# Kernel optimization log

Measured on AMD Instinct MI355X. Metric: run time of the kernel, lower is better.

The kernel has to match this reference:

```python
import jax, jax.numpy as jnp
import numpy as np

TAU = 2.0
BN_EPS = 1e-5
SG_ALPHA = 4.0  # spikingjelly default sigmoid surrogate alpha

@jax.custom_vjp
def heaviside(x):
    return (x >= 0).astype(x.dtype)

def _h_fwd(x):
    return heaviside(x), x

def _h_bwd(x, g):
    sg = jax.nn.sigmoid(SG_ALPHA * x)
    return (SG_ALPHA * sg * (1.0 - sg) * g,)

heaviside.defvjp(_h_fwd, _h_bwd)

def lif(x, v_th):
    # x: (T, ...). LIFNode defaults: tau=2, decay_input=True, v_reset=0 (hard reset).
    def step(v, xt):
        v = v + (xt - v) / TAU
        s = heaviside(v - v_th)
        return v * (1.0 - s), s
    _, spikes = jax.lax.scan(step, jnp.zeros_like(x[0]), x)
    return spikes

def bn(x, gamma, beta, mean, var):
    # x: (T,B,D,V), channel axis = 2; inference-mode BatchNorm1d
    inv = gamma * jax.lax.rsqrt(var + BN_EPS)
    return x * inv[None, None, :, None] + (beta - mean * inv)[None, None, :, None]

def conv1x1(W, x):
    # W: (out,in), x: (T,B,D,V)
    return jnp.einsum('od,tbdv->tbov', W, x)

def setup_inputs() -> dict:
    key = jax.random.key(0)
    T, B, D, V = 4, 64, 512, 256
    ks = jax.random.split(key, 4)
    s = 1.0 / np.sqrt(D)
    return {
        'x': jax.random.normal(ks[0], (T, B, D, V), jnp.float32),
        'Wq': jax.random.normal(ks[1], (D, D), jnp.float32) * s,
        'q_gamma': jnp.ones((D,), jnp.float32), 'q_beta': jnp.zeros((D,), jnp.float32),
        'q_mean': jnp.zeros((D,), jnp.float32), 'q_var': jnp.ones((D,), jnp.float32),
        'Wk': jax.random.normal(ks[2], (D, D), jnp.float32) * s,
        'k_gamma': jnp.ones((D,), jnp.float32), 'k_beta': jnp.zeros((D,), jnp.float32),
        'k_mean': jnp.zeros((D,), jnp.float32), 'k_var': jnp.ones((D,), jnp.float32),
        'Wp': jax.random.normal(ks[3], (D, D), jnp.float32) * s,
        'p_gamma': jnp.ones((D,), jnp.float32), 'p_beta': jnp.zeros((D,), jnp.float32),
        'p_mean': jnp.zeros((D,), jnp.float32), 'p_var': jnp.ones((D,), jnp.float32),
    }

def reference(x, Wq, q_gamma, q_beta, q_mean, q_var,
              Wk, k_gamma, k_beta, k_mean, k_var,
              Wp, p_gamma, p_beta, p_mean, p_var):
    T, B, D, V = x.shape
    H = 4
    hd = D // H
    q = lif(bn(conv1x1(Wq, x), q_gamma, q_beta, q_mean, q_var), 1.0)
    k = lif(bn(conv1x1(Wk, x), k_gamma, k_beta, k_mean, k_var), 1.0)
    qh = q.reshape(T, B, H, hd, V)
    kh = k.reshape(T, B, H, hd, V)
    q_sum = qh.sum(axis=3, keepdims=True)        # (T,B,H,1,V)
    gate = lif(q_sum, 0.5)                        # attn_lif, threshold 0.5
    out = (gate * kh).reshape(T, B, D, V)
    out2 = lif(bn(conv1x1(Wp, out), p_gamma, p_beta, p_mean, p_var), 1.0)
    return out2
```

## Files before the change

kernel.cpp:

```cpp
#include <hip/hip_runtime.h>

#define T_ 4
#define B_ 64
#define D_ 512
#define V_ 256

#define XSH   0ull
#define XSM   67108864ull
#define XSL   134217728ull
#define OUTBT 201326592ull
#define WT    268435456ull
#define BNOF  273154048ull

typedef unsigned short u16;
typedef __attribute__((ext_vector_type(8))) __bf16 bf16x8;
typedef __attribute__((ext_vector_type(4))) float f32x4;
typedef __attribute__((ext_vector_type(8))) unsigned short u16x8;
typedef __attribute__((ext_vector_type(4))) unsigned short u16x4;

__device__ __forceinline__ u16 f2bf(float f) {
    unsigned u = __float_as_uint(f);
    return (u16)((u + 0x7FFFu + ((u >> 16) & 1u)) >> 16);
}
__device__ __forceinline__ float bf2f(u16 h) {
    return __uint_as_float(((unsigned)h) << 16);
}

__global__ __launch_bounds__(256) void k_prep2(
    const float* __restrict__ Wq, const float* __restrict__ Wk, const float* __restrict__ Wp,
    const float* __restrict__ qg, const float* __restrict__ qb,
    const float* __restrict__ qm, const float* __restrict__ qv,
    const float* __restrict__ kg, const float* __restrict__ kb,
    const float* __restrict__ km, const float* __restrict__ kv,
    const float* __restrict__ pg, const float* __restrict__ pb,
    const float* __restrict__ pm, const float* __restrict__ pv,
    char* __restrict__ ws)
{
    const int g = blockIdx.x * 256 + threadIdx.x;
    const int mat = g >> 15;
    const int r = g & 32767;
    const int lane = r & 63;
    const int q = r >> 6;
    const int ip = q & 7;
    const int q2 = q >> 3;
    const int it = q2 & 15;
    const int head = q2 >> 4;
    const int row = head * 128 + ip * 16 + (lane & 15);
    const int kcol = it * 32 + (lane >> 4) * 8;
    const float* W = (mat == 0) ? Wq : (mat == 1 ? Wk : Wp);

    u16x8 h8, m8, l8;
#pragma unroll
    for (int e = 0; e < 8; ++e) {
        const float f = W[row * 512 + kcol + e];
        const u16 h = f2bf(f);          const float fh = bf2f(h);
        const u16 m = f2bf(f - fh);     const float fm = bf2f(m);
        const u16 l = f2bf(f - fh - fm);
        h8[e] = h; m8[e] = m; l8[e] = l;
    }
    u16* wt = (u16*)(ws + WT);
    const size_t o = (size_t)r * 8;
    *(u16x8*)(wt + (size_t)(mat * 3 + 0) * 262144 + o) = h8;
    *(u16x8*)(wt + (size_t)(mat * 3 + 1) * 262144 + o) = m8;
    *(u16x8*)(wt + (size_t)(mat * 3 + 2) * 262144 + o) = l8;

    if (g < 512) {
        float* bn = (float*)(ws + BNOF);
        float iv;
        iv = qg[g] * (1.0f / sqrtf(qv[g] + 1e-5f)); bn[g]        = iv; bn[512  + g] = qb[g] - qm[g] * iv;
        iv = kg[g] * (1.0f / sqrtf(kv[g] + 1e-5f)); bn[1024 + g] = iv; bn[1536 + g] = kb[g] - km[g] * iv;
        iv = pg[g] * (1.0f / sqrtf(pv[g] + 1e-5f)); bn[2048 + g] = iv; bn[2560 + g] = pb[g] - pm[g] * iv;
    }
}

__global__ __launch_bounds__(256) void k_split_x2(
    const float* __restrict__ x, char* __restrict__ ws)
{
    const int bt = blockIdx.x >> 4;
    const int it = blockIdx.x & 15;
    const int tid = threadIdx.x;
#pragma unroll
    for (int r2 = 0; r2 < 4; ++r2) {
        const int slot = r2 * 256 + tid;
        const int vg = slot >> 6;
        const int ll = slot & 63;
        const int v  = vg * 16 + (ll & 15);
        const int d0 = it * 32 + (ll >> 4) * 8;
        u16x8 h8, m8, l8;
#pragma unroll
        for (int e = 0; e < 8; ++e) {
            const float f = x[(size_t)bt * 131072 + (size_t)(d0 + e) * 256 + v];
            const u16 h = f2bf(f);          const float fh = bf2f(h);
            const u16 m = f2bf(f - fh);     const float fm = bf2f(m);
            const u16 lo = f2bf(f - fh - fm);
            h8[e] = h; m8[e] = m; l8[e] = lo;
        }
        const size_t o = (size_t)bt * 262144ull + (size_t)it * 16384ull
                       + (size_t)vg * 1024ull + (size_t)ll * 16ull;
        *(u16x8*)(ws + XSH + o) = h8;
        *(u16x8*)(ws + XSM + o) = m8;
        *(u16x8*)(ws + XSL + o) = l8;
    }
}

__global__ __launch_bounds__(512, 2) void k_qk2(char* __restrict__ ws)
{
    __shared__ u16 tile[32768];
    __shared__ float qs[2][256];
    __shared__ float gatef[4][256];

    const int tid  = threadIdx.x;
    const int lane = tid & 63;
    const int wave = tid >> 6;
    const int wr = wave >> 2;
    const int wc = wave & 3;
    const int quad = lane >> 4;
    const int l15  = lane & 15;

    const int xcd  = blockIdx.x & 7;
    const int slot = blockIdx.x >> 3;
    const int b    = xcd * 8 + (slot >> 2);
    const int head = slot & 3;

    constexpr int PA[6] = {0, 0, 1, 1, 0, 2};
    constexpr int PB[6] = {0, 1, 0, 1, 2, 0};

    float gstate = 0.f;

    for (int ph = 0; ph < 2; ++ph) {
        const size_t abase = WT + (size_t)ph * 3ull * 524288ull
                           + (size_t)head * 131072ull
                           + (size_t)wr * 4096ull + (size_t)lane * 16ull;
        const float* bn = (const float*)(ws + BNOF + (size_t)ph * 4096);

        f32x4 st[4][4];
#pragma unroll
        for (int i = 0; i < 4; ++i)
#pragma unroll
            for (int j = 0; j < 4; ++j) st[i][j] = (f32x4){0.f, 0.f, 0.f, 0.f};

        for (int t = 0; t < 4; ++t) {
            const int bt = t * 64 + b;
            const size_t bbase = (size_t)bt * 262144ull
                               + (size_t)(wc * 4) * 1024ull + (size_t)lane * 16ull;
            f32x4 acc[4][4];
#pragma unroll
            for (int i = 0; i < 4; ++i)
#pragma unroll
                for (int j = 0; j < 4; ++j) acc[i][j] = (f32x4){0.f, 0.f, 0.f, 0.f};

#pragma unroll 4
            for (int it = 0; it < 16; ++it) {
                bf16x8 afr[3][4];
#pragma unroll
                for (int s = 0; s < 3; ++s)
#pragma unroll
                    for (int i = 0; i < 4; ++i)
                        afr[s][i] = *(const bf16x8*)(ws + abase + (size_t)s * 524288ull
                                      + (size_t)it * 8192ull + (size_t)i * 1024ull);
#pragma unroll
                for (int j = 0; j < 4; ++j) {
                    bf16x8 bfr[3];
#pragma unroll
                    for (int s = 0; s < 3; ++s)
                        bfr[s] = *(const bf16x8*)(ws + (size_t)s * 67108864ull + bbase
                                   + (size_t)it * 16384ull + (size_t)j * 1024ull);
#pragma unroll
                    for (int i = 0; i < 4; ++i)
#pragma unroll
                        for (int p = 0; p < 6; ++p)
                            acc[i][j] = __builtin_amdgcn_mfma_f32_16x16x32_bf16(
                                afr[PA[p]][i], bfr[PB[p]], acc[i][j], 0, 0, 0);
                }
            }

            if (ph == 0) {
                float qp[4] = {0.f, 0.f, 0.f, 0.f};
#pragma unroll
                for (int i = 0; i < 4; ++i) {
                    const int ob = head * 128 + wr * 64 + i * 16 + quad * 4;
                    const f32x4 inv = *(const f32x4*)(bn + ob);
                    const f32x4 add = *(const f32x4*)(bn + 512 + ob);
#pragma unroll
                    for (int j = 0; j < 4; ++j)
#pragma unroll
                        for (int r = 0; r < 4; ++r) {
                            const float y = acc[i][j][r] * inv[r] + add[r];
                            float v = (st[i][j][r] + y) * 0.5f;
                            const float s = (v >= 1.0f) ? 1.f : 0.f;
                            st[i][j][r] = (v >= 1.0f) ? 0.f : v;
                            qp[j] += s;
                        }
                }
#pragma unroll
                for (int j = 0; j < 4; ++j) {
                    qp[j] += __shfl_xor(qp[j], 16, 64);
                    qp[j] += __shfl_xor(qp[j], 32, 64);
                }
                if (quad == 0) {
#pragma unroll
                    for (int j = 0; j < 4; ++j)
                        qs[wr][wc * 64 + j * 16 + l15] = qp[j];
                }
                __syncthreads();
                if (tid < 256) {
                    const float qsum = qs[0][tid] + qs[1][tid];
                    gstate = (gstate + qsum) * 0.5f;
                    const float gt = (gstate >= 0.5f) ? 1.f : 0.f;
                    gstate = (gstate >= 0.5f) ? 0.f : gstate;
                    gatef[t][tid] = gt;
                }
                __syncthreads();
            } else {
#pragma unroll
                for (int i = 0; i < 4; ++i) {
                    const int ob = head * 128 + wr * 64 + i * 16 + quad * 4;
                    const f32x4 inv = *(const f32x4*)(bn + ob);
                    const f32x4 add = *(const f32x4*)(bn + 512 + ob);
                    const int itL = wr * 2 + (i >> 1);
                    const int ls  = ((i & 1) * 2 + (quad >> 1)) * 16 + l15;
                    const int e0  = (quad & 1) * 4;
#pragma unroll
                    for (int j = 0; j < 4; ++j) {
                        const int col = wc * 64 + j * 16 + l15;
                        const float gt = gatef[t][col];
                        u16x4 w;
#pragma unroll
                        for (int r = 0; r < 4; ++r) {
                            const float y = acc[i][j][r] * inv[r] + add[r];
                            float v = (st[i][j][r] + y) * 0.5f;
                            const float s = (v >= 1.0f) ? 1.f : 0.f;
                            st[i][j][r] = (v >= 1.0f) ? 0.f : v;
                            w[r] = (s * gt != 0.f) ? (u16)0x3F80 : (u16)0;
                        }
                        *(u16x4*)&tile[(size_t)((itL * 16 + wc * 4 + j) * 64 + ls) * 8 + e0] = w;
                    }
                }
                __syncthreads();
                const size_t dst = OUTBT + ((size_t)bt * 16ull + (size_t)head * 4ull) * 16384ull;
#pragma unroll
                for (int c = 0; c < 8; ++c) {
                    const int idx = c * 512 + tid;
                    *(float4*)(ws + dst + (size_t)idx * 16) = *(const float4*)&tile[(size_t)idx * 8];
                }
                __syncthreads();
            }
        }
    }
}

__global__ __launch_bounds__(512, 2) void k_p2(char* __restrict__ ws,
                                               float* __restrict__ out2)
{
    const int tid  = threadIdx.x;
    const int lane = tid & 63;
    const int wave = tid >> 6;
    const int wr = wave >> 2;
    const int wc = wave & 3;
    const int quad = lane >> 4;
    const int l15  = lane & 15;

    const int xcd  = blockIdx.x & 7;
    const int slot = blockIdx.x >> 3;
    const int b  = xcd * 8 + (slot >> 2);
    const int ot = slot & 3;

    const size_t abase = WT + 6ull * 524288ull + (size_t)ot * 131072ull
                       + (size_t)wr * 4096ull + (size_t)lane * 16ull;
    const float* bn = (const float*)(ws + BNOF + 8192);

    f32x4 st[4][4];
#pragma unroll
    for (int i = 0; i < 4; ++i)
#pragma unroll
        for (int j = 0; j < 4; ++j) st[i][j] = (f32x4){0.f, 0.f, 0.f, 0.f};

    for (int t = 0; t < 4; ++t) {
        const int bt = t * 64 + b;
        const size_t bbase = OUTBT + (size_t)bt * 262144ull
                           + (size_t)(wc * 4) * 1024ull + (size_t)lane * 16ull;
        f32x4 acc[4][4];
#pragma unroll
        for (int i = 0; i < 4; ++i)
#pragma unroll
            for (int j = 0; j < 4; ++j) acc[i][j] = (f32x4){0.f, 0.f, 0.f, 0.f};

#pragma unroll 4
        for (int it = 0; it < 16; ++it) {
            bf16x8 afr[3][4];
#pragma unroll
            for (int s = 0; s < 3; ++s)
#pragma unroll
                for (int i = 0; i < 4; ++i)
                    afr[s][i] = *(const bf16x8*)(ws + abase + (size_t)s * 524288ull
                                  + (size_t)it * 8192ull + (size_t)i * 1024ull);
#pragma unroll
            for (int j = 0; j < 4; ++j) {
                const bf16x8 bfr = *(const bf16x8*)(ws + bbase
                                     + (size_t)it * 16384ull + (size_t)j * 1024ull);
#pragma unroll
                for (int i = 0; i < 4; ++i)
#pragma unroll
                    for (int p = 0; p < 3; ++p)
                        acc[i][j] = __builtin_amdgcn_mfma_f32_16x16x32_bf16(
                            afr[p][i], bfr, acc[i][j], 0, 0, 0);
            }
        }

#pragma unroll
        for (int i = 0; i < 4; ++i) {
            const int ob = ot * 128 + wr * 64 + i * 16 + quad * 4;
            const f32x4 inv = *(const f32x4*)(bn + ob);
            const f32x4 add = *(const f32x4*)(bn + 512 + ob);
#pragma unroll
            for (int j = 0; j < 4; ++j) {
                const int col = wc * 64 + j * 16 + l15;
#pragma unroll
                for (int r = 0; r < 4; ++r) {
                    const float y = acc[i][j][r] * inv[r] + add[r];
                    float v = (st[i][j][r] + y) * 0.5f;
                    const float s = (v >= 1.0f) ? 1.f : 0.f;
                    st[i][j][r] = (v >= 1.0f) ? 0.f : v;
                    out2[((size_t)(t * 64 + b) * 512 + ob + r) * 256 + col] = s;
                }
            }
        }
    }
}

extern "C" void kernel_launch(void* const* d_in, const int* in_sizes, int n_in,
                              void* d_out, int out_size, void* d_ws, size_t ws_size,
                              hipStream_t stream)
{
    const float* x  = (const float*)d_in[0];
    const float* Wq = (const float*)d_in[1];
    const float* qg = (const float*)d_in[2];
    const float* qb = (const float*)d_in[3];
    const float* qm = (const float*)d_in[4];
    const float* qv = (const float*)d_in[5];
    const float* Wk = (const float*)d_in[6];
    const float* kg = (const float*)d_in[7];
    const float* kb = (const float*)d_in[8];
    const float* km = (const float*)d_in[9];
    const float* kv = (const float*)d_in[10];
    const float* Wp = (const float*)d_in[11];
    const float* pg = (const float*)d_in[12];
    const float* pb = (const float*)d_in[13];
    const float* pm = (const float*)d_in[14];
    const float* pv = (const float*)d_in[15];

    char* ws = (char*)d_ws;

    k_prep2<<<384, 256, 0, stream>>>(Wq, Wk, Wp, qg, qb, qm, qv,
                                     kg, kb, km, kv, pg, pb, pm, pv, ws);

    k_split_x2<<<4096, 256, 0, stream>>>(x, ws);

    k_qk2<<<256, 512, 0, stream>>>(ws);

    k_p2<<<256, 512, 0, stream>>>(ws, (float*)d_out);
}
```

Before: 711.4 us.

## Process two timesteps per pass to reuse weight fragments across GEMMs

Both fused GEMM kernels now handle timesteps in pairs. Each weight (A) fragment loaded from global memory feeds MFMAs for two timesteps' activations, which halves weight reloads and gives more independent MFMA chains. The cost is a second 4x4 accumulator set, roughly doubling accumulator registers, which could cause spills or lower occupancy under launch_bounds(512,2). The unroll factor drops from 4 to 2 to compensate, and the LIF epilogues still run sequentially per timestep.

```diff
diff --git a/kernel.cpp b/kernel.cpp
--- a/kernel.cpp
+++ b/kernel.cpp
@@ -139,17 +139,98 @@
 #pragma unroll
             for (int j = 0; j < 4; ++j) st[i][j] = (f32x4){0.f, 0.f, 0.f, 0.f};
 
-        for (int t = 0; t < 4; ++t) {
-            const int bt = t * 64 + b;
-            const size_t bbase = (size_t)bt * 262144ull
-                               + (size_t)(wc * 4) * 1024ull + (size_t)lane * 16ull;
-            f32x4 acc[4][4];
+        auto epi_q = [&](int t, f32x4 (&acc)[4][4]) {
+            float qp[4] = {0.f, 0.f, 0.f, 0.f};
+#pragma unroll
+            for (int i = 0; i < 4; ++i) {
+                const int ob = head * 128 + wr * 64 + i * 16 + quad * 4;
+                const f32x4 inv = *(const f32x4*)(bn + ob);
+                const f32x4 add = *(const f32x4*)(bn + 512 + ob);
+#pragma unroll
+                for (int j = 0; j < 4; ++j)
+#pragma unroll
+                    for (int r = 0; r < 4; ++r) {
+                        const float y = acc[i][j][r] * inv[r] + add[r];
+                        float v = (st[i][j][r] + y) * 0.5f;
+                        const float s = (v >= 1.0f) ? 1.f : 0.f;
+                        st[i][j][r] = (v >= 1.0f) ? 0.f : v;
+                        qp[j] += s;
+                    }
+            }
+#pragma unroll
+            for (int j = 0; j < 4; ++j) {
+                qp[j] += __shfl_xor(qp[j], 16, 64);
+                qp[j] += __shfl_xor(qp[j], 32, 64);
+            }
+            if (quad == 0) {
+#pragma unroll
+                for (int j = 0; j < 4; ++j)
+                    qs[wr][wc * 64 + j * 16 + l15] = qp[j];
+            }
+            __syncthreads();
+            if (tid < 256) {
+                const float qsum = qs[0][tid] + qs[1][tid];
+                gstate = (gstate + qsum) * 0.5f;
+                const float gt = (gstate >= 0.5f) ? 1.f : 0.f;
+                gstate = (gstate >= 0.5f) ? 0.f : gstate;
+                gatef[t][tid] = gt;
+            }
+            __syncthreads();
+        };
+
+        auto epi_k = [&](int t, int bt, f32x4 (&acc)[4][4]) {
+#pragma unroll
+            for (int i = 0; i < 4; ++i) {
+                const int ob = head * 128 + wr * 64 + i * 16 + quad * 4;
+                const f32x4 inv = *(const f32x4*)(bn + ob);
+                const f32x4 add = *(const f32x4*)(bn + 512 + ob);
+                const int itL = wr * 2 + (i >> 1);
+                const int ls  = ((i & 1) * 2 + (quad >> 1)) * 16 + l15;
+                const int e0  = (quad & 1) * 4;
+#pragma unroll
+                for (int j = 0; j < 4; ++j) {
+                    const int col = wc * 64 + j * 16 + l15;
+                    const float gt = gatef[t][col];
+                    u16x4 w;
+#pragma unroll
+                    for (int r = 0; r < 4; ++r) {
+                        const float y = acc[i][j][r] * inv[r] + add[r];
+                        float v = (st[i][j][r] + y) * 0.5f;
+                        const float s = (v >= 1.0f) ? 1.f : 0.f;
+                        st[i][j][r] = (v >= 1.0f) ? 0.f : v;
+                        w[r] = (s * gt != 0.f) ? (u16)0x3F80 : (u16)0;
+                    }
+                    *(u16x4*)&tile[(size_t)((itL * 16 + wc * 4 + j) * 64 + ls) * 8 + e0] = w;
+                }
+            }
+            __syncthreads();
+            const size_t dst = OUTBT + ((size_t)bt * 16ull + (size_t)head * 4ull) * 16384ull;
+#pragma unroll
+            for (int c = 0; c < 8; ++c) {
+                const int idx = c * 512 + tid;
+                *(float4*)(ws + dst + (size_t)idx * 16) = *(const float4*)&tile[(size_t)idx * 8];
+            }
+            __syncthreads();
+        };
+
+        for (int tp = 0; tp < 2; ++tp) {
+            const int ta = tp * 2, tb = tp * 2 + 1;
+            const int bta = ta * 64 + b, btb = tb * 64 + b;
+            const size_t bbaseA = (size_t)bta * 262144ull
+                                + (size_t)(wc * 4) * 1024ull + (size_t)lane * 16ull;
+            const size_t bbaseB = (size_t)btb * 262144ull
+                                + (size_t)(wc * 4) * 1024ull + (size_t)lane * 16ull;
+
+            f32x4 acc0[4][4], acc1[4][4];
 #pragma unroll
             for (int i = 0; i < 4; ++i)
 #pragma unroll
-                for (int j = 0; j < 4; ++j) acc[i][j] = (f32x4){0.f, 0.f, 0.f, 0.f};
-
-#pragma unroll 4
+                for (int j = 0; j < 4; ++j) {
+                    acc0[i][j] = (f32x4){0.f, 0.f, 0.f, 0.f};
+                    acc1[i][j] = (f32x4){0.f, 0.f, 0.f, 0.f};
+                }
+
+#pragma unroll 2
             for (int it = 0; it < 16; ++it) {
                 bf16x8 afr[3][4];
 #pragma unroll
@@ -160,90 +241,32 @@
                                       + (size_t)it * 8192ull + (size_t)i * 1024ull);
 #pragma unroll
                 for (int j = 0; j < 4; ++j) {
-                    bf16x8 bfr[3];
-#pragma unroll
-                    for (int s = 0; s < 3; ++s)
-                        bfr[s] = *(const bf16x8*)(ws + (size_t)s * 67108864ull + bbase
+                    bf16x8 b0[3], b1[3];
+#pragma unroll
+                    for (int s = 0; s < 3; ++s) {
+                        b0[s] = *(const bf16x8*)(ws + (size_t)s * 67108864ull + bbaseA
                                    + (size_t)it * 16384ull + (size_t)j * 1024ull);
+                        b1[s] = *(const bf16x8*)(ws + (size_t)s * 67108864ull + bbaseB
+                                   + (size_t)it * 16384ull + (size_t)j * 1024ull);
+                    }
 #pragma unroll
                     for (int i = 0; i < 4; ++i)
 #pragma unroll
-                        for (int p = 0; p < 6; ++p)
-                            acc[i][j] = __builtin_amdgcn_mfma_f32_16x16x32_bf16(
-                                afr[PA[p]][i], bfr[PB[p]], acc[i][j], 0, 0, 0);
-                }
-            }
-
-            if (ph == 0) {
-                float qp[4] = {0.f, 0.f, 0.f, 0.f};
-#pragma unroll
-                for (int i = 0; i < 4; ++i) {
-                    const int ob = head * 128 + wr * 64 + i * 16 + quad * 4;
-                    const f32x4 inv = *(const f32x4*)(bn + ob);
-                    const f32x4 add = *(const f32x4*)(bn + 512 + ob);
-#pragma unroll
-                    for (int j = 0; j < 4; ++j)
-#pragma unroll
-                        for (int r = 0; r < 4; ++r) {
-                            const float y = acc[i][j][r] * inv[r] + add[r];
-                            float v = (st[i][j][r] + y) * 0.5f;
-                            const float s = (v >= 1.0f) ? 1.f : 0.f;
-                            st[i][j][r] = (v >= 1.0f) ? 0.f : v;
-                            qp[j] += s;
+                        for (int p = 0; p < 6; ++p) {
+                            acc0[i][j] = __builtin_amdgcn_mfma_f32_16x16x32_bf16(
+                                afr[PA[p]][i], b0[PB[p]], acc0[i][j], 0, 0, 0);
+                            acc1[i][j] = __builtin_amdgcn_mfma_f32_16x16x32_bf16(
+                                afr[PA[p]][i], b1[PB[p]], acc1[i][j], 0, 0, 0);
                         }
                 }
-#pragma unroll
-                for (int j = 0; j < 4; ++j) {
-                    qp[j] += __shfl_xor(qp[j], 16, 64);
-                    qp[j] += __shfl_xor(qp[j], 32, 64);
-                }
-                if (quad == 0) {
-#pragma unroll
-                    for (int j = 0; j < 4; ++j)
-                        qs[wr][wc * 64 + j * 16 + l15] = qp[j];
-                }
-                __syncthreads();
-                if (tid < 256) {
-                    const float qsum = qs[0][tid] + qs[1][tid];
-                    gstate = (gstate + qsum) * 0.5f;
-                    const float gt = (gstate >= 0.5f) ? 1.f : 0.f;
-                    gstate = (gstate >= 0.5f) ? 0.f : gstate;
-                    gatef[t][tid] = gt;
-                }
-                __syncthreads();
+            }
+
+            if (ph == 0) {
+                epi_q(ta, acc0);
+                epi_q(tb, acc1);
             } else {
-#pragma unroll
-                for (int i = 0; i < 4; ++i) {
-                    const int ob = head * 128 + wr * 64 + i * 16 + quad * 4;
-                    const f32x4 inv = *(const f32x4*)(bn + ob);
-                    const f32x4 add = *(const f32x4*)(bn + 512 + ob);
-                    const int itL = wr * 2 + (i >> 1);
-                    const int ls  = ((i & 1) * 2 + (quad >> 1)) * 16 + l15;
-                    const int e0  = (quad & 1) * 4;
-#pragma unroll
-                    for (int j = 0; j < 4; ++j) {
-                        const int col = wc * 64 + j * 16 + l15;
-                        const float gt = gatef[t][col];
-                        u16x4 w;
-#pragma unroll
-                        for (int r = 0; r < 4; ++r) {
-                            const float y = acc[i][j][r] * inv[r] + add[r];
-                            float v = (st[i][j][r] + y) * 0.5f;
-                            const float s = (v >= 1.0f) ? 1.f : 0.f;
-                            st[i][j][r] = (v >= 1.0f) ? 0.f : v;
-                            w[r] = (s * gt != 0.f) ? (u16)0x3F80 : (u16)0;
-                        }
-                        *(u16x4*)&tile[(size_t)((itL * 16 + wc * 4 + j) * 64 + ls) * 8 + e0] = w;
-                    }
-                }
-                __syncthreads();
-                const size_t dst = OUTBT + ((size_t)bt * 16ull + (size_t)head * 4ull) * 16384ull;
-#pragma unroll
-                for (int c = 0; c < 8; ++c) {
-                    const int idx = c * 512 + tid;
-                    *(float4*)(ws + dst + (size_t)idx * 16) = *(const float4*)&tile[(size_t)idx * 8];
-                }
-                __syncthreads();
+                epi_k(ta, bta, acc0);
+                epi_k(tb, btb, acc1);
             }
         }
     }
@@ -275,38 +298,7 @@
 #pragma unroll
         for (int j = 0; j < 4; ++j) st[i][j] = (f32x4){0.f, 0.f, 0.f, 0.f};
 
-    for (int t = 0; t < 4; ++t) {
-        const int bt = t * 64 + b;
-        const size_t bbase = OUTBT + (size_t)bt * 262144ull
-                           + (size_t)(wc * 4) * 1024ull + (size_t)lane * 16ull;
-        f32x4 acc[4][4];
-#pragma unroll
-        for (int i = 0; i < 4; ++i)
-#pragma unroll
-            for (int j = 0; j < 4; ++j) acc[i][j] = (f32x4){0.f, 0.f, 0.f, 0.f};
-
-#pragma unroll 4
-        for (int it = 0; it < 16; ++it) {
-            bf16x8 afr[3][4];
-#pragma unroll
-            for (int s = 0; s < 3; ++s)
-#pragma unroll
-                for (int i = 0; i < 4; ++i)
-                    afr[s][i] = *(const bf16x8*)(ws + abase + (size_t)s * 524288ull
-                                  + (size_t)it * 8192ull + (size_t)i * 1024ull);
-#pragma unroll
-            for (int j = 0; j < 4; ++j) {
-                const bf16x8 bfr = *(const bf16x8*)(ws + bbase
-                                     + (size_t)it * 16384ull + (size_t)j * 1024ull);
-#pragma unroll
-                for (int i = 0; i < 4; ++i)
-#pragma unroll
-                    for (int p = 0; p < 3; ++p)
-                        acc[i][j] = __builtin_amdgcn_mfma_f32_16x16x32_bf16(
-                            afr[p][i], bfr, acc[i][j], 0, 0, 0);
-            }
-        }
-
+    auto epi = [&](int t, f32x4 (&acc)[4][4]) {
 #pragma unroll
         for (int i = 0; i < 4; ++i) {
             const int ob = ot * 128 + wr * 64 + i * 16 + quad * 4;
@@ -325,6 +317,54 @@
                 }
             }
         }
+    };
+
+    for (int tp = 0; tp < 2; ++tp) {
+        const int ta = tp * 2, tb = tp * 2 + 1;
+        const int bta = ta * 64 + b, btb = tb * 64 + b;
+        const size_t bbaseA = OUTBT + (size_t)bta * 262144ull
+                            + (size_t)(wc * 4) * 1024ull + (size_t)lane * 16ull;
+        const size_t bbaseB = OUTBT + (size_t)btb * 262144ull
+                            + (size_t)(wc * 4) * 1024ull + (size_t)lane * 16ull;
+
+        f32x4 acc0[4][4], acc1[4][4];
+#pragma unroll
+        for (int i = 0; i < 4; ++i)
+#pragma unroll
+            for (int j = 0; j < 4; ++j) {
+                acc0[i][j] = (f32x4){0.f, 0.f, 0.f, 0.f};
+                acc1[i][j] = (f32x4){0.f, 0.f, 0.f, 0.f};
+            }
+
+#pragma unroll 2
+        for (int it = 0; it < 16; ++it) {
+            bf16x8 afr[3][4];
+#pragma unroll
+            for (int s = 0; s < 3; ++s)
+#pragma unroll
+                for (int i = 0; i < 4; ++i)
+                    afr[s][i] = *(const bf16x8*)(ws + abase + (size_t)s * 524288ull
+                                  + (size_t)it * 8192ull + (size_t)i * 1024ull);
+#pragma unroll
+            for (int j = 0; j < 4; ++j) {
+                const bf16x8 b0 = *(const bf16x8*)(ws + bbaseA
+                                     + (size_t)it * 16384ull + (size_t)j * 1024ull);
+                const bf16x8 b1 = *(const bf16x8*)(ws + bbaseB
+                                     + (size_t)it * 16384ull + (size_t)j * 1024ull);
+#pragma unroll
+                for (int i = 0; i < 4; ++i)
+#pragma unroll
+                    for (int p = 0; p < 3; ++p) {
+                        acc0[i][j] = __builtin_amdgcn_mfma_f32_16x16x32_bf16(
+                            afr[p][i], b0, acc0[i][j], 0, 0, 0);
+                        acc1[i][j] = __builtin_amdgcn_mfma_f32_16x16x32_bf16(
+                            afr[p][i], b1, acc1[i][j], 0, 0, 0);
+                    }
+            }
+        }
+
+        epi(ta, acc0);
+        epi(tb, acc1);
     }
 }
 
```

Result: slower. 750.4 us (+5.5%).

## Stage GEMM operands through double-buffered LDS with async global-to-LDS loads

Applied to the files above, without the earlier changes.

Both GEMM kernels now stage weight and activation tiles into shared memory using global_load_lds direct loads, double-buffered so the next k-slice is fetched while the current one feeds MFMA. Previously each wave loaded fragments straight from global memory, so the same data was re-read by several waves with no cross-wave reuse. The large LDS footprint forces occupancy down to one block per CU and adds two barriers per iteration, which could limit latency hiding.

```diff
diff --git a/kernel.cpp b/kernel.cpp
--- a/kernel.cpp
+++ b/kernel.cpp
@@ -25,6 +25,11 @@
 __device__ __forceinline__ float bf2f(u16 h) {
     return __uint_as_float(((unsigned)h) << 16);
 }
+
+#define GLL16(g, l) __builtin_amdgcn_global_load_lds( \
+    (const __attribute__((address_space(1))) void*)(g), \
+    (__attribute__((address_space(3))) void*)(l), 16, 0, 0)
+#define WAITVM(n) asm volatile("s_waitcnt vmcnt(" #n ")" ::: "memory")
 
 __global__ __launch_bounds__(256) void k_prep2(
     const float* __restrict__ Wq, const float* __restrict__ Wk, const float* __restrict__ Wp,
@@ -103,11 +108,12 @@
     }
 }
 
-__global__ __launch_bounds__(512, 2) void k_qk2(char* __restrict__ ws)
+__global__ __launch_bounds__(512, 1) void k_qk2(char* __restrict__ ws)
 {
-    __shared__ u16 tile[32768];
-    __shared__ float qs[2][256];
-    __shared__ float gatef[4][256];
+    __shared__ char lds[153600];
+    u16*   tile  = (u16*)lds;
+    float* qs    = (float*)(lds + 147456);
+    float* gatef = (float*)(lds + 149504);
 
     const int tid  = threadIdx.x;
     const int lane = tid & 63;
@@ -116,6 +122,7 @@
     const int wc = wave & 3;
     const int quad = lane >> 4;
     const int l15  = lane & 15;
+    const int to   = tid * 16;
 
     const int xcd  = blockIdx.x & 7;
     const int slot = blockIdx.x >> 3;
@@ -128,9 +135,7 @@
     float gstate = 0.f;
 
     for (int ph = 0; ph < 2; ++ph) {
-        const size_t abase = WT + (size_t)ph * 3ull * 524288ull
-                           + (size_t)head * 131072ull
-                           + (size_t)wr * 4096ull + (size_t)lane * 16ull;
+        const size_t wbase = WT + (size_t)ph * 3ull * 524288ull + (size_t)head * 131072ull;
         const float* bn = (const float*)(ws + BNOF + (size_t)ph * 4096);
 
         f32x4 st[4][4];
@@ -141,30 +146,61 @@
 
         for (int t = 0; t < 4; ++t) {
             const int bt = t * 64 + b;
-            const size_t bbase = (size_t)bt * 262144ull
-                               + (size_t)(wc * 4) * 1024ull + (size_t)lane * 16ull;
+            const size_t btbase = (size_t)bt * 262144ull;
+
             f32x4 acc[4][4];
 #pragma unroll
             for (int i = 0; i < 4; ++i)
 #pragma unroll
                 for (int j = 0; j < 4; ++j) acc[i][j] = (f32x4){0.f, 0.f, 0.f, 0.f};
 
-#pragma unroll 4
+#pragma unroll
+            for (int s = 0; s < 3; ++s)
+                GLL16(ws + wbase + (size_t)s * 524288ull + to,
+                      lds + s * 8192 + to);
+#pragma unroll
+            for (int s = 0; s < 3; ++s)
+#pragma unroll
+                for (int h = 0; h < 2; ++h)
+                    GLL16(ws + (size_t)s * 67108864ull + btbase + h * 8192 + to,
+                          lds + 24576 + s * 16384 + h * 8192 + to);
+
+#pragma unroll 2
             for (int it = 0; it < 16; ++it) {
+                char* buf = lds + (it & 1) * 73728;
+                if (it < 15) {
+                    char* nbuf = lds + ((it + 1) & 1) * 73728;
+                    const size_t itn = (size_t)(it + 1);
+#pragma unroll
+                    for (int s = 0; s < 3; ++s)
+                        GLL16(ws + wbase + (size_t)s * 524288ull + itn * 8192ull + to,
+                              nbuf + s * 8192 + to);
+#pragma unroll
+                    for (int s = 0; s < 3; ++s)
+#pragma unroll
+                        for (int h = 0; h < 2; ++h)
+                            GLL16(ws + (size_t)s * 67108864ull + btbase + itn * 16384ull + h * 8192 + to,
+                                  nbuf + 24576 + s * 16384 + h * 8192 + to);
+                    WAITVM(9);
+                } else {
+                    WAITVM(0);
+                }
+                __builtin_amdgcn_s_barrier();
+
                 bf16x8 afr[3][4];
 #pragma unroll
                 for (int s = 0; s < 3; ++s)
 #pragma unroll
                     for (int i = 0; i < 4; ++i)
-                        afr[s][i] = *(const bf16x8*)(ws + abase + (size_t)s * 524288ull
-                                      + (size_t)it * 8192ull + (size_t)i * 1024ull);
+                        afr[s][i] = *(const bf16x8*)(buf + s * 8192 + wr * 4096
+                                                     + i * 1024 + lane * 16);
 #pragma unroll
                 for (int j = 0; j < 4; ++j) {
                     bf16x8 bfr[3];
 #pragma unroll
                     for (int s = 0; s < 3; ++s)
-                        bfr[s] = *(const bf16x8*)(ws + (size_t)s * 67108864ull + bbase
-                                   + (size_t)it * 16384ull + (size_t)j * 1024ull);
+                        bfr[s] = *(const bf16x8*)(buf + 24576 + s * 16384
+                                                  + (wc * 4 + j) * 1024 + lane * 16);
 #pragma unroll
                     for (int i = 0; i < 4; ++i)
 #pragma unroll
@@ -172,6 +208,7 @@
                             acc[i][j] = __builtin_amdgcn_mfma_f32_16x16x32_bf16(
                                 afr[PA[p]][i], bfr[PB[p]], acc[i][j], 0, 0, 0);
                 }
+                __builtin_amdgcn_s_barrier();
             }
 
             if (ph == 0) {
@@ -200,15 +237,15 @@
                 if (quad == 0) {
 #pragma unroll
                     for (int j = 0; j < 4; ++j)
-                        qs[wr][wc * 64 + j * 16 + l15] = qp[j];
+                        qs[wr * 256 + wc * 64 + j * 16 + l15] = qp[j];
                 }
                 __syncthreads();
                 if (tid < 256) {
-                    const float qsum = qs[0][tid] + qs[1][tid];
+                    const float qsum = qs[tid] + qs[256 + tid];
                     gstate = (gstate + qsum) * 0.5f;
                     const float gt = (gstate >= 0.5f) ? 1.f : 0.f;
                     gstate = (gstate >= 0.5f) ? 0.f : gstate;
-                    gatef[t][tid] = gt;
+                    gatef[t * 256 + tid] = gt;
                 }
                 __syncthreads();
             } else {
@@ -223,7 +260,7 @@
 #pragma unroll
                     for (int j = 0; j < 4; ++j) {
                         const int col = wc * 64 + j * 16 + l15;
-                        const float gt = gatef[t][col];
+                        const float gt = gatef[t * 256 + col];
                         u16x4 w;
 #pragma unroll
                         for (int r = 0; r < 4; ++r) {
@@ -249,9 +286,11 @@
     }
 }
 
-__global__ __launch_bounds__(512, 2) void k_p2(char* __restrict__ ws,
+__global__ __launch_bounds__(512, 1) void k_p2(char* __restrict__ ws,
                                                float* __restrict__ out2)
 {
+    __shared__ char lds[81920];
+
     const int tid  = threadIdx.x;
     const int lane = tid & 63;
     const int wave = tid >> 6;
@@ -259,14 +298,14 @@
     const int wc = wave & 3;
     const int quad = lane >> 4;
     const int l15  = lane & 15;
+    const int to   = tid * 16;
 
     const int xcd  = blockIdx.x & 7;
     const int slot = blockIdx.x >> 3;
     const int b  = xcd * 8 + (slot >> 2);
     const int ot = slot & 3;
 
-    const size_t abase = WT + 6ull * 524288ull + (size_t)ot * 131072ull
-                       + (size_t)wr * 4096ull + (size_t)lane * 16ull;
+    const size_t wbase = WT + 6ull * 524288ull + (size_t)ot * 131072ull;
     const float* bn = (const float*)(ws + BNOF + 8192);
 
     f32x4 st[4][4];
@@ -277,27 +316,54 @@
 
     for (int t = 0; t < 4; ++t) {
         const int bt = t * 64 + b;
-        const size_t bbase = OUTBT + (size_t)bt * 262144ull
-                           + (size_t)(wc * 4) * 1024ull + (size_t)lane * 16ull;
+        const size_t btbase = OUTBT + (size_t)bt * 262144ull;
+
         f32x4 acc[4][4];
 #pragma unroll
         for (int i = 0; i < 4; ++i)
 #pragma unroll
             for (int j = 0; j < 4; ++j) acc[i][j] = (f32x4){0.f, 0.f, 0.f, 0.f};
 
-#pragma unroll 4
+#pragma unroll
+        for (int s = 0; s < 3; ++s)
+            GLL16(ws + wbase + (size_t)s * 524288ull + to,
+                  lds + s * 8192 + to);
+#pragma unroll
+        for (int h = 0; h < 2; ++h)
+            GLL16(ws + btbase + h * 8192 + to,
+                  lds + 24576 + h * 8192 + to);
+
+#pragma unroll 2
         for (int it = 0; it < 16; ++it) {
+            char* buf = lds + (it & 1) * 40960;
+            if (it < 15) {
+                char* nbuf = lds + ((it + 1) & 1) * 40960;
+                const size_t itn = (size_t)(it + 1);
+#pragma unroll
+                for (int s = 0; s < 3; ++s)
+                    GLL16(ws + wbase + (size_t)s * 524288ull + itn * 8192ull + to,
+                          nbuf + s * 8192 + to);
+#pragma unroll
+                for (int h = 0; h < 2; ++h)
+                    GLL16(ws + btbase + itn * 16384ull + h * 8192 + to,
+                          nbuf + 24576 + h * 8192 + to);
+                WAITVM(5);
+            } else {
+                WAITVM(0);
+            }
+            __builtin_amdgcn_s_barrier();
+
             bf16x8 afr[3][4];
 #pragma unroll
             for (int s = 0; s < 3; ++s)
 #pragma unroll
                 for (int i = 0; i < 4; ++i)
-                    afr[s][i] = *(const bf16x8*)(ws + abase + (size_t)s * 524288ull
-                                  + (size_t)it * 8192ull + (size_t)i * 1024ull);
+                    afr[s][i] = *(const bf16x8*)(buf + s * 8192 + wr * 4096
+                                                 + i * 1024 + lane * 16);
 #pragma unroll
             for (int j = 0; j < 4; ++j) {
-                const bf16x8 bfr = *(const bf16x8*)(ws + bbase
-                                     + (size_t)it * 16384ull + (size_t)j * 1024ull);
+                const bf16x8 bfr = *(const bf16x8*)(buf + 24576
+                                                    + (wc * 4 + j) * 1024 + lane * 16);
 #pragma unroll
                 for (int i = 0; i < 4; ++i)
 #pragma unroll
@@ -305,6 +371,7 @@
                         acc[i][j] = __builtin_amdgcn_mfma_f32_16x16x32_bf16(
                             afr[p][i], bfr, acc[i][j], 0, 0, 0);
             }
+            __builtin_amdgcn_s_barrier();
         }
 
 #pragma unroll
@@ -325,6 +392,7 @@
                 }
             }
         }
+        WAITVM(0);
     }
 }
 
```

After: 656.7 us. -7.7%, faster.

## Stage GEMM operands through double-buffered LDS with async global-to-LDS loads

Applied to the files above, without the earlier changes.

Both GEMM kernels now copy A (weights) and B (activations) tiles into LDS with global_load_lds. The buffers are double-buffered, so the next K-step's loads are issued while the current step's MFMAs run, replacing direct per-wave global loads. Coordination uses vmcnt waits, raw s_barrier and setprio around MFMA blocks. The q/k output tile is written straight to global instead of staged through LDS. The larger LDS footprint drops occupancy to one block per CU, and correctness now depends on hand-tuned waitcnt counts.

```diff
diff --git a/kernel.cpp b/kernel.cpp
--- a/kernel.cpp
+++ b/kernel.cpp
@@ -25,6 +25,12 @@
 __device__ __forceinline__ float bf2f(u16 h) {
     return __uint_as_float(((unsigned)h) << 16);
 }
+
+#define GLL16(g, l) __builtin_amdgcn_global_load_lds( \
+    (const __attribute__((address_space(1))) void*)(g), \
+    (__attribute__((address_space(3))) void*)(l), 16, 0, 0)
+#define WAITVM(n) asm volatile("s_waitcnt vmcnt(" #n ")" ::: "memory")
+#define WAITLGKM() asm volatile("s_waitcnt lgkmcnt(0)" ::: "memory")
 
 __global__ __launch_bounds__(256) void k_prep2(
     const float* __restrict__ Wq, const float* __restrict__ Wk, const float* __restrict__ Wp,
@@ -103,11 +109,11 @@
     }
 }
 
-__global__ __launch_bounds__(512, 2) void k_qk2(char* __restrict__ ws)
+__global__ __launch_bounds__(512, 1) void k_qk2(char* __restrict__ ws)
 {
-    __shared__ u16 tile[32768];
-    __shared__ float qs[2][256];
-    __shared__ float gatef[4][256];
+    __shared__ char lds[150528];
+    float* qs    = (float*)(lds + 147456);
+    float* gatef = (float*)(lds + 149504);
 
     const int tid  = threadIdx.x;
     const int lane = tid & 63;
@@ -116,6 +122,9 @@
     const int wc = wave & 3;
     const int quad = lane >> 4;
     const int l15  = lane & 15;
+    const int to   = tid * 16;
+    const int offB0 = (wc * 4 + 0 + wr) * 1024 + lane * 16;
+    const int offB1 = (wc * 4 + 2 + wr) * 1024 + lane * 16;
 
     const int xcd  = blockIdx.x & 7;
     const int slot = blockIdx.x >> 3;
@@ -125,55 +134,81 @@
     constexpr int PA[6] = {0, 0, 1, 1, 0, 2};
     constexpr int PB[6] = {0, 1, 0, 1, 2, 0};
 
+#define QK_ISSUE_A(gg, nb) { \
+    const size_t wb_ = WT + (size_t)((gg) >> 6) * 1572864ull \
+                     + (size_t)head * 131072ull + (size_t)((gg) & 15) * 8192ull; \
+    _Pragma("unroll") \
+    for (int s_ = 0; s_ < 3; ++s_) \
+        GLL16(ws + wb_ + (size_t)s_ * 524288ull + to, (nb) + s_ * 8192 + to); }
+
+#define QK_ISSUE_B(gg, nb, off) { \
+    const size_t bb_ = (size_t)(((((gg) >> 4) & 3) * 64 + b)) * 262144ull \
+                     + (size_t)((gg) & 15) * 16384ull; \
+    _Pragma("unroll") \
+    for (int s_ = 0; s_ < 3; ++s_) \
+        GLL16(ws + (size_t)s_ * 67108864ull + bb_ + (off), (nb) + 24576 + s_ * 16384 + (off)); }
+
+#define QK_DO_J(jq) { \
+    bf16x8 bfr[3]; \
+    _Pragma("unroll") \
+    for (int s_ = 0; s_ < 3; ++s_) \
+        bfr[s_] = *(const bf16x8*)(buf + 24576 + s_ * 16384 + (wc * 4 + (jq)) * 1024 + lane * 16); \
+    __builtin_amdgcn_s_setprio(1); \
+    _Pragma("unroll") \
+    for (int i_ = 0; i_ < 4; ++i_) \
+        _Pragma("unroll") \
+        for (int p_ = 0; p_ < 6; ++p_) \
+            acc[i_][jq] = __builtin_amdgcn_mfma_f32_16x16x32_bf16( \
+                afr[PA[p_]][i_], bfr[PB[p_]], acc[i_][jq], 0, 0, 0); \
+    __builtin_amdgcn_s_setprio(0); }
+
+    f32x4 st[4][4], acc[4][4];
     float gstate = 0.f;
 
-    for (int ph = 0; ph < 2; ++ph) {
-        const size_t abase = WT + (size_t)ph * 3ull * 524288ull
-                           + (size_t)head * 131072ull
-                           + (size_t)wr * 4096ull + (size_t)lane * 16ull;
+    QK_ISSUE_A(0, lds);
+    QK_ISSUE_B(0, lds, offB0);
+    QK_ISSUE_B(0, lds, offB1);
+
+#pragma unroll 1
+    for (int g = 0; g < 128; ++g) {
+        const int ph = g >> 6;
+        const int t  = (g >> 4) & 3;
+        const int it = g & 15;
+        char* buf  = lds + (g & 1) * 73728;
+        char* nbuf = lds + ((g + 1) & 1) * 73728;
+        const bool kepi = (ph == 1) && (it == 15);
         const float* bn = (const float*)(ws + BNOF + (size_t)ph * 4096);
 
-        f32x4 st[4][4];
-#pragma unroll
-        for (int i = 0; i < 4; ++i)
-#pragma unroll
-            for (int j = 0; j < 4; ++j) st[i][j] = (f32x4){0.f, 0.f, 0.f, 0.f};
-
-        for (int t = 0; t < 4; ++t) {
-            const int bt = t * 64 + b;
-            const size_t bbase = (size_t)bt * 262144ull
-                               + (size_t)(wc * 4) * 1024ull + (size_t)lane * 16ull;
-            f32x4 acc[4][4];
+        if (it == 0) {
 #pragma unroll
             for (int i = 0; i < 4; ++i)
 #pragma unroll
-                for (int j = 0; j < 4; ++j) acc[i][j] = (f32x4){0.f, 0.f, 0.f, 0.f};
-
-#pragma unroll 4
-            for (int it = 0; it < 16; ++it) {
-                bf16x8 afr[3][4];
-#pragma unroll
-                for (int s = 0; s < 3; ++s)
-#pragma unroll
-                    for (int i = 0; i < 4; ++i)
-                        afr[s][i] = *(const bf16x8*)(ws + abase + (size_t)s * 524288ull
-                                      + (size_t)it * 8192ull + (size_t)i * 1024ull);
-#pragma unroll
                 for (int j = 0; j < 4; ++j) {
-                    bf16x8 bfr[3];
-#pragma unroll
-                    for (int s = 0; s < 3; ++s)
-                        bfr[s] = *(const bf16x8*)(ws + (size_t)s * 67108864ull + bbase
-                                   + (size_t)it * 16384ull + (size_t)j * 1024ull);
-#pragma unroll
-                    for (int i = 0; i < 4; ++i)
-#pragma unroll
-                        for (int p = 0; p < 6; ++p)
-                            acc[i][j] = __builtin_amdgcn_mfma_f32_16x16x32_bf16(
-                                afr[PA[p]][i], bfr[PB[p]], acc[i][j], 0, 0, 0);
-                }
-            }
-
+                    acc[i][j] = (f32x4){0.f, 0.f, 0.f, 0.f};
+                    if (t == 0) st[i][j] = (f32x4){0.f, 0.f, 0.f, 0.f};
+                }
+        }
+
+        WAITVM(3);
+        __builtin_amdgcn_s_barrier();
+        if (!kepi) QK_ISSUE_A(g + 1, nbuf);
+        bf16x8 afr[3][4];
+#pragma unroll
+        for (int s = 0; s < 3; ++s)
+#pragma unroll
+            for (int i = 0; i < 4; ++i)
+                afr[s][i] = *(const bf16x8*)(buf + s * 8192 + wr * 4096
+                                             + i * 1024 + lane * 16);
+        QK_DO_J(0);
+        if (!kepi) QK_ISSUE_B(g + 1, nbuf, offB0);
+        QK_DO_J(1);
+        if (kepi) { WAITVM(0); } else { WAITVM(6); }
+        __builtin_amdgcn_s_barrier();
+        if (!kepi) QK_ISSUE_B(g + 1, nbuf, offB1);
+        QK_DO_J(2);
+        QK_DO_J(3);
+
+        if (it == 15) {
             if (ph == 0) {
                 float qp[4] = {0.f, 0.f, 0.f, 0.f};
 #pragma unroll
@@ -200,18 +235,22 @@
                 if (quad == 0) {
 #pragma unroll
                     for (int j = 0; j < 4; ++j)
-                        qs[wr][wc * 64 + j * 16 + l15] = qp[j];
-                }
-                __syncthreads();
+                        qs[wr * 256 + wc * 64 + j * 16 + l15] = qp[j];
+                }
+                WAITLGKM();
+                __builtin_amdgcn_s_barrier();
                 if (tid < 256) {
-                    const float qsum = qs[0][tid] + qs[1][tid];
+                    const float qsum = qs[tid] + qs[256 + tid];
                     gstate = (gstate + qsum) * 0.5f;
                     const float gt = (gstate >= 0.5f) ? 1.f : 0.f;
                     gstate = (gstate >= 0.5f) ? 0.f : gstate;
-                    gatef[t][tid] = gt;
-                }
-                __syncthreads();
+                    gatef[t * 256 + tid] = gt;
+                }
+                WAITLGKM();
+                __builtin_amdgcn_s_barrier();
             } else {
+                const int bt = t * 64 + b;
+                const size_t dst = OUTBT + ((size_t)bt * 16ull + (size_t)head * 4ull) * 16384ull;
 #pragma unroll
                 for (int i = 0; i < 4; ++i) {
                     const int ob = head * 128 + wr * 64 + i * 16 + quad * 4;
@@ -223,7 +262,7 @@
 #pragma unroll
                     for (int j = 0; j < 4; ++j) {
                         const int col = wc * 64 + j * 16 + l15;
-                        const float gt = gatef[t][col];
+                        const float gt = gatef[t * 256 + col];
                         u16x4 w;
 #pragma unroll
                         for (int r = 0; r < 4; ++r) {
@@ -233,25 +272,28 @@
                             st[i][j][r] = (v >= 1.0f) ? 0.f : v;
                             w[r] = (s * gt != 0.f) ? (u16)0x3F80 : (u16)0;
                         }
-                        *(u16x4*)&tile[(size_t)((itL * 16 + wc * 4 + j) * 64 + ls) * 8 + e0] = w;
+                        *(u16x4*)(ws + dst
+                            + (size_t)((itL * 16 + wc * 4 + j) * 64 + ls) * 16 + e0 * 2) = w;
                     }
                 }
-                __syncthreads();
-                const size_t dst = OUTBT + ((size_t)bt * 16ull + (size_t)head * 4ull) * 16384ull;
-#pragma unroll
-                for (int c = 0; c < 8; ++c) {
-                    const int idx = c * 512 + tid;
-                    *(float4*)(ws + dst + (size_t)idx * 16) = *(const float4*)&tile[(size_t)idx * 8];
-                }
-                __syncthreads();
+                if (g != 127) {
+                    QK_ISSUE_A(g + 1, nbuf);
+                    QK_ISSUE_B(g + 1, nbuf, offB0);
+                    QK_ISSUE_B(g + 1, nbuf, offB1);
+                }
             }
         }
     }
-}
-
-__global__ __launch_bounds__(512, 2) void k_p2(char* __restrict__ ws,
+#undef QK_ISSUE_A
+#undef QK_ISSUE_B
+#undef QK_DO_J
+}
+
+__global__ __launch_bounds__(512, 1) void k_p2(char* __restrict__ ws,
                                                float* __restrict__ out2)
 {
+    __shared__ char lds[81920];
+
     const int tid  = threadIdx.x;
     const int lane = tid & 63;
     const int wave = tid >> 6;
@@ -259,73 +301,112 @@
     const int wc = wave & 3;
     const int quad = lane >> 4;
     const int l15  = lane & 15;
+    const int to   = tid * 16;
+    const int offB0 = (wc * 4 + 0 + wr) * 1024 + lane * 16;
+    const int offB1 = (wc * 4 + 2 + wr) * 1024 + lane * 16;
 
     const int xcd  = blockIdx.x & 7;
     const int slot = blockIdx.x >> 3;
     const int b  = xcd * 8 + (slot >> 2);
     const int ot = slot & 3;
 
-    const size_t abase = WT + 6ull * 524288ull + (size_t)ot * 131072ull
-                       + (size_t)wr * 4096ull + (size_t)lane * 16ull;
     const float* bn = (const float*)(ws + BNOF + 8192);
 
-    f32x4 st[4][4];
-#pragma unroll
-    for (int i = 0; i < 4; ++i)
-#pragma unroll
-        for (int j = 0; j < 4; ++j) st[i][j] = (f32x4){0.f, 0.f, 0.f, 0.f};
-
-    for (int t = 0; t < 4; ++t) {
-        const int bt = t * 64 + b;
-        const size_t bbase = OUTBT + (size_t)bt * 262144ull
-                           + (size_t)(wc * 4) * 1024ull + (size_t)lane * 16ull;
-        f32x4 acc[4][4];
-#pragma unroll
-        for (int i = 0; i < 4; ++i)
-#pragma unroll
-            for (int j = 0; j < 4; ++j) acc[i][j] = (f32x4){0.f, 0.f, 0.f, 0.f};
-
-#pragma unroll 4
-        for (int it = 0; it < 16; ++it) {
-            bf16x8 afr[3][4];
-#pragma unroll
-            for (int s = 0; s < 3; ++s)
-#pragma unroll
-                for (int i = 0; i < 4; ++i)
-                    afr[s][i] = *(const bf16x8*)(ws + abase + (size_t)s * 524288ull
-                                  + (size_t)it * 8192ull + (size_t)i * 1024ull);
-#pragma unroll
-            for (int j = 0; j < 4; ++j) {
-                const bf16x8 bfr = *(const bf16x8*)(ws + bbase
-                                     + (size_t)it * 16384ull + (size_t)j * 1024ull);
-#pragma unroll
-                for (int i = 0; i < 4; ++i)
-#pragma unroll
-                    for (int p = 0; p < 3; ++p)
-                        acc[i][j] = __builtin_amdgcn_mfma_f32_16x16x32_bf16(
-                            afr[p][i], bfr, acc[i][j], 0, 0, 0);
+#define P_ISSUE_A(gg, nb) { \
+    const size_t wb_ = WT + 6ull * 524288ull + (size_t)ot * 131072ull \
+                     + (size_t)((gg) & 15) * 8192ull; \
+    _Pragma("unroll") \
+    for (int s_ = 0; s_ < 3; ++s_) \
+        GLL16(ws + wb_ + (size_t)s_ * 524288ull + to, (nb) + s_ * 8192 + to); }
+
+#define P_ISSUE_B(gg, nb, off) { \
+    const size_t bb_ = OUTBT + (size_t)((((gg) >> 4) * 64) + b) * 262144ull \
+                     + (size_t)((gg) & 15) * 16384ull; \
+    GLL16(ws + bb_ + (off), (nb) + 24576 + (off)); }
+
+#define P_DO_J(jq) { \
+    const bf16x8 bfr = *(const bf16x8*)(buf + 24576 + (wc * 4 + (jq)) * 1024 + lane * 16); \
+    __builtin_amdgcn_s_setprio(1); \
+    _Pragma("unroll") \
+    for (int i_ = 0; i_ < 4; ++i_) \
+        _Pragma("unroll") \
+        for (int p_ = 0; p_ < 3; ++p_) \
+            acc[i_][jq] = __builtin_amdgcn_mfma_f32_16x16x32_bf16( \
+                afr[p_][i_], bfr, acc[i_][jq], 0, 0, 0); \
+    __builtin_amdgcn_s_setprio(0); }
+
+    f32x4 st[4][4], acc[4][4];
+
+    P_ISSUE_A(0, lds);
+    P_ISSUE_B(0, lds, offB0);
+    P_ISSUE_B(0, lds, offB1);
+
+#pragma unroll 1
+    for (int g = 0; g < 64; ++g) {
+        const int t  = g >> 4;
+        const int it = g & 15;
+        char* buf  = lds + (g & 1) * 40960;
+        char* nbuf = lds + ((g + 1) & 1) * 40960;
+        const bool kepi = (it == 15);
+
+        if (it == 0) {
+#pragma unroll
+            for (int i = 0; i < 4; ++i)
+#pragma unroll
+                for (int j = 0; j < 4; ++j) {
+                    acc[i][j] = (f32x4){0.f, 0.f, 0.f, 0.f};
+                    if (g == 0) st[i][j] = (f32x4){0.f, 0.f, 0.f, 0.f};
+                }
+        }
+
+        WAITVM(1);
+        __builtin_amdgcn_s_barrier();
+        if (!kepi) P_ISSUE_A(g + 1, nbuf);
+        bf16x8 afr[3][4];
+#pragma unroll
+        for (int s = 0; s < 3; ++s)
+#pragma unroll
+            for (int i = 0; i < 4; ++i)
+                afr[s][i] = *(const bf16x8*)(buf + s * 8192 + wr * 4096
+                                             + i * 1024 + lane * 16);
+        P_DO_J(0);
+        if (!kepi) P_ISSUE_B(g + 1, nbuf, offB0);
+        P_DO_J(1);
+        if (kepi) { WAITVM(0); } else { WAITVM(4); }
+        __builtin_amdgcn_s_barrier();
+        if (!kepi) P_ISSUE_B(g + 1, nbuf, offB1);
+        P_DO_J(2);
+        P_DO_J(3);
+
+        if (kepi) {
+#pragma unroll
+            for (int i = 0; i < 4; ++i) {
+                const int ob = ot * 128 + wr * 64 + i * 16 + quad * 4;
+                const f32x4 inv = *(const f32x4*)(bn + ob);
+                const f32x4 add = *(const f32x4*)(bn + 512 + ob);
+#pragma unroll
+                for (int j = 0; j < 4; ++j) {
+                    const int col = wc * 64 + j * 16 + l15;
+#pragma unroll
+                    for (int r = 0; r < 4; ++r) {
+                        const float y = acc[i][j][r] * inv[r] + add[r];
+                        float v = (st[i][j][r] + y) * 0.5f;
+                        const float s = (v >= 1.0f) ? 1.f : 0.f;
+                        st[i][j][r] = (v >= 1.0f) ? 0.f : v;
+                        out2[((size_t)(t * 64 + b) * 512 + ob + r) * 256 + col] = s;
+                    }
+                }
             }
-        }
-
-#pragma unroll
-        for (int i = 0; i < 4; ++i) {
-            const int ob = ot * 128 + wr * 64 + i * 16 + quad * 4;
-            const f32x4 inv = *(const f32x4*)(bn + ob);
-            const f32x4 add = *(const f32x4*)(bn + 512 + ob);
-#pragma unroll
-            for (int j = 0; j < 4; ++j) {
-                const int col = wc * 64 + j * 16 + l15;
-#pragma unroll
-                for (int r = 0; r < 4; ++r) {
-                    const float y = acc[i][j][r] * inv[r] + add[r];
-                    float v = (st[i][j][r] + y) * 0.5f;
-                    const float s = (v >= 1.0f) ? 1.f : 0.f;
-                    st[i][j][r] = (v >= 1.0f) ? 0.f : v;
-                    out2[((size_t)(t * 64 + b) * 512 + ob + r) * 256 + col] = s;
-                }
+            if (g != 63) {
+                P_ISSUE_A(g + 1, nbuf);
+                P_ISSUE_B(g + 1, nbuf, offB0);
+                P_ISSUE_B(g + 1, nbuf, offB1);
             }
         }
     }
+#undef P_ISSUE_A
+#undef P_ISSUE_B
+#undef P_DO_J
 }
 
 extern "C" void kernel_launch(void* const* d_in, const int* in_sizes, int n_in,
```

Measured after the change: 683.9 us. 3.9% less time.
